# Performance work log

Measured on AMD Instinct MI355X. Metric: run time of the kernel, lower is better.

The kernel has to match this reference:

```python
import jax, jax.numpy as jnp
import numpy as np

D_MODEL = 1024
NUM_HEADS = 16
D_K = D_MODEL // NUM_HEADS
BATCH = 4
SEQ = 1024
NEG_INF = jnp.float32(-1e30)


def setup_inputs() -> dict:
    key = jax.random.key(0)
    ks = jax.random.split(key, 12)
    s = 1.0 / np.sqrt(D_MODEL)
    inp = {
        "Q": jax.random.normal(ks[0], (BATCH, SEQ, D_MODEL), jnp.float32),
        "K": jax.random.normal(ks[1], (BATCH, SEQ, D_MODEL), jnp.float32),
        "V": jax.random.normal(ks[2], (BATCH, SEQ, D_MODEL), jnp.float32),
        # causal mask, broadcastable [1,1,Sq,Sk]; entries==0 are masked out
        "mask": jnp.tril(jnp.ones((SEQ, SEQ), jnp.int32))[None, None],
        "W_q": jax.random.normal(ks[3], (D_MODEL, D_MODEL), jnp.float32) * s,
        "b_q": jnp.zeros((D_MODEL,), jnp.float32),
        "W_k": jax.random.normal(ks[4], (D_MODEL, D_MODEL), jnp.float32) * s,
        "b_k": jnp.zeros((D_MODEL,), jnp.float32),
        "W_v": jax.random.normal(ks[5], (D_MODEL, D_MODEL), jnp.float32) * s,
        "b_v": jnp.zeros((D_MODEL,), jnp.float32),
        "W_o": jax.random.normal(ks[6], (D_MODEL, D_MODEL), jnp.float32) * s,
        "b_o": jnp.zeros((D_MODEL,), jnp.float32),
    }
    return inp


def _split_heads(x):
    b, s, _ = x.shape
    return x.reshape(b, s, NUM_HEADS, D_K).transpose(0, 2, 1, 3)  # [b,h,s,dk]


def reference(Q, K, V, mask, W_q, b_q, W_k, b_k, W_v, b_v, W_o, b_o):
    # linear projections (torch Linear: x @ W.T + b)
    q = _split_heads(Q @ W_q.T + b_q)
    k = _split_heads(K @ W_k.T + b_k)
    v = _split_heads(V @ W_v.T + b_v)
    scale = 1.0 / jnp.sqrt(jnp.float32(D_K))
    scores = jnp.einsum("bhqd,bhkd->bhqk", q, k) * scale
    scores = jnp.where(mask == 0, NEG_INF, scores)
    attn = jax.nn.softmax(scores, axis=-1)  # dropout is identity in eval mode
    out = jnp.einsum("bhqk,bhkd->bhqd", attn, v)
    out = out.transpose(0, 2, 1, 3).reshape(Q.shape[0], Q.shape[1], D_MODEL)
    out = out @ W_o.T + b_o
    return out, attn
```

## Files before the change

kernel.cpp:

```cpp
#include <hip/hip_runtime.h>
#include <math.h>

#define SEQ 1024
#define DM  1024

typedef unsigned short u16;
typedef __attribute__((ext_vector_type(8))) short bf16x8;
typedef __attribute__((ext_vector_type(8))) unsigned short u16x8;
typedef __attribute__((ext_vector_type(4))) float f32x4;

__device__ __forceinline__ u16 f2bf(float f) {
  union { float f; unsigned int u; } x; x.f = f;
  return (u16)((x.u + 0x7fffu + ((x.u >> 16) & 1u)) >> 16);
}

__device__ __forceinline__ void gload16(const void* g, void* l) {
  __builtin_amdgcn_global_load_lds(
      (const __attribute__((address_space(1))) unsigned int*)g,
      (__attribute__((address_space(3))) unsigned int*)l, 16, 0, 0);
}

struct ConvArgs { const float* s[7]; u16* d[7]; };

__global__ __launch_bounds__(256) void conv_bf16(ConvArgs a) {
  const long long t  = (long long)blockIdx.x * 256 + threadIdx.x;
  const long long e0 = t * 8;
  const int u   = (int)(e0 >> 20);
  const int seg = (u < 12) ? (u >> 2) : (u - 9);
  const long long base = (u < 12) ? ((long long)(u >> 2) << 22) : ((long long)u << 20);
  const long long off  = e0 - base;
  const float* sp = a.s[seg] + off;
  float4 x = *(const float4*)sp;
  float4 y = *(const float4*)(sp + 4);
  u16x8 o;
  o[0]=f2bf(x.x); o[1]=f2bf(x.y); o[2]=f2bf(x.z); o[3]=f2bf(x.w);
  o[4]=f2bf(y.x); o[5]=f2bf(y.y); o[6]=f2bf(y.z); o[7]=f2bf(y.w);
  *(u16x8*)(a.d[seg] + off) = o;
}

struct GemmJob  { const u16* X; const u16* W; const float* bias; void* out; int mode; float scale; };
struct GemmJobs { GemmJob j[3]; };

__global__ __launch_bounds__(256) void gemm_bt(GemmJobs jobs) {
  __shared__ u16 As[8192];
  __shared__ u16 Bs[8192];
  const GemmJob job = jobs.j[blockIdx.z];
  const int tid  = threadIdx.x;
  const int wave = tid >> 6, lane = tid & 63;
  const int lm = lane & 15, qd = lane >> 4;
  const int wm = wave & 1,  wn = wave >> 1;
  const int tm = blockIdx.x * 128, tn = blockIdx.y * 128;

  f32x4 acc[4][4];
  #pragma unroll
  for (int i = 0; i < 4; i++)
    #pragma unroll
    for (int jx = 0; jx < 4; jx++) { f32x4 z = {0.f,0.f,0.f,0.f}; acc[i][jx] = z; }

  for (int kt = 0; kt < 1024; kt += 64) {
    #pragma unroll
    for (int i = 0; i < 4; i++) {
      const int s = (wave * 4 + i) * 64 + lane;
      const int r = s >> 3;
      const int c = (s & 7) ^ (r & 7);
      gload16(job.X + (size_t)(tm + r) * 1024 + kt + c * 8, As + (wave * 4 + i) * 512);
      gload16(job.W + (size_t)(tn + r) * 1024 + kt + c * 8, Bs + (wave * 4 + i) * 512);
    }
    __syncthreads();
    #pragma unroll
    for (int ks = 0; ks < 2; ks++) {
      bf16x8 af[4], bf[4];
      #pragma unroll
      for (int i = 0; i < 4; i++) {
        const int ra = wm * 64 + i * 16 + lm;
        af[i] = *(const bf16x8*)&As[ra * 64 + ((((ks << 2) | qd)) ^ (ra & 7)) * 8];
        const int rb = wn * 64 + i * 16 + lm;
        bf[i] = *(const bf16x8*)&Bs[rb * 64 + ((((ks << 2) | qd)) ^ (rb & 7)) * 8];
      }
      #pragma unroll
      for (int mi = 0; mi < 4; mi++)
        #pragma unroll
        for (int ni = 0; ni < 4; ni++)
          acc[mi][ni] = __builtin_amdgcn_mfma_f32_16x16x32_bf16(af[mi], bf[ni], acc[mi][ni], 0, 0, 0);
    }
    __syncthreads();
  }

  #pragma unroll
  for (int ni = 0; ni < 4; ni++) {
    const int n = tn + wn * 64 + ni * 16 + lm;
    const float bn = job.bias[n];
    #pragma unroll
    for (int mi = 0; mi < 4; mi++) {
      #pragma unroll
      for (int r = 0; r < 4; r++) {
        const int m = tm + wm * 64 + mi * 16 + (qd << 2) + r;
        const float v = (acc[mi][ni][r] + bn) * job.scale;
        if (job.mode == 0) {
          const int b = m >> 10, s = m & 1023, h = n >> 6, d = n & 63;
          ((u16*)job.out)[((size_t)((b << 4) + h) * 1024 + s) * 64 + d] = f2bf(v);
        } else if (job.mode == 1) {
          const int b = m >> 10, s = m & 1023, h = n >> 6, d = n & 63;
          ((u16*)job.out)[((size_t)((b << 4) + h) * 64 + d) * 1024 + s] = f2bf(v);
        } else {
          ((float*)job.out)[(size_t)m * 1024 + n] = v;
        }
      }
    }
  }
}

__global__ __launch_bounds__(256)
void attn_pass1(const u16* __restrict__ qbuf, const u16* __restrict__ kbuf,
                const u16* __restrict__ vtbuf, float* __restrict__ Linv,
                u16* __restrict__ ctx, float* __restrict__ attn) {
  __shared__ u16 P[4][512];
  const int tid = threadIdx.x, wave = tid >> 6, lane = tid & 63;
  const int bh = blockIdx.y;

  if (blockIdx.x >= 16) {
    const int b  = blockIdx.x - 16;
    const int L4 = (15 - b) * 16;
    float* base = attn + (size_t)bh * SEQ * SEQ + (size_t)(b * 64) * SEQ + (b + 1) * 64;
    const f32x4 z = {0.f, 0.f, 0.f, 0.f};
    for (int r = 0; r < 64; ++r) {
      f32x4* rowp = (f32x4*)(base + (size_t)r * SEQ);
      for (int s = tid; s < L4; s += 256) rowp[s] = z;
    }
    return;
  }

  const int lm = lane & 15, qd = lane >> 4;
  const int qt = blockIdx.x * 4 + wave;
  const int q0 = qt * 16;
  const u16* Q  = qbuf  + (size_t)bh * SEQ * 64;
  const u16* K  = kbuf  + (size_t)bh * SEQ * 64;
  const u16* VT = vtbuf + (size_t)bh * 64 * SEQ;

  const bf16x8 qa = *(const bf16x8*)(Q + (size_t)(q0 + lm) * 64 + qd * 8);
  const bf16x8 qb = *(const bf16x8*)(Q + (size_t)(q0 + lm) * 64 + 32 + qd * 8);

  f32x4 o[4];
  float lsum[4] = {0.f, 0.f, 0.f, 0.f};
  #pragma unroll
  for (int i = 0; i < 4; i++) { f32x4 z = {0.f,0.f,0.f,0.f}; o[i] = z; }
  u16* Pw = P[wave];

  for (int kt = 0; kt < q0 + 16; kt += 32) {
    const u16* k0p = K + (size_t)(kt + lm) * 64 + qd * 8;
    const u16* k1p = K + (size_t)(kt + 16 + lm) * 64 + qd * 8;
    const bf16x8 k0a = *(const bf16x8*)k0p;
    const bf16x8 k0b = *(const bf16x8*)(k0p + 32);
    const bf16x8 k1a = *(const bf16x8*)k1p;
    const bf16x8 k1b = *(const bf16x8*)(k1p + 32);
    f32x4 s0 = {0.f,0.f,0.f,0.f}, s1 = {0.f,0.f,0.f,0.f};
    s0 = __builtin_amdgcn_mfma_f32_16x16x32_bf16(qa, k0a, s0, 0, 0, 0);
    s0 = __builtin_amdgcn_mfma_f32_16x16x32_bf16(qb, k0b, s0, 0, 0, 0);
    s1 = __builtin_amdgcn_mfma_f32_16x16x32_bf16(qa, k1a, s1, 0, 0, 0);
    s1 = __builtin_amdgcn_mfma_f32_16x16x32_bf16(qb, k1b, s1, 0, 0, 0);
    #pragma unroll
    for (int r = 0; r < 4; r++) {
      const int row = q0 + (qd << 2) + r;
      const float e0 = (kt + lm      <= row) ? __expf(s0[r]) : 0.f;
      const float e1 = (kt + 16 + lm <= row) ? __expf(s1[r]) : 0.f;
      lsum[r] += e0 + e1;
      Pw[((qd << 2) + r) * 32 + lm]      = f2bf(e0);
      Pw[((qd << 2) + r) * 32 + 16 + lm] = f2bf(e1);
    }
    const bf16x8 pf = *(const bf16x8*)&Pw[lm * 32 + qd * 8];
    #pragma unroll
    for (int db = 0; db < 4; db++) {
      const bf16x8 vf = *(const bf16x8*)(VT + (size_t)(db * 16 + lm) * SEQ + kt + qd * 8);
      o[db] = __builtin_amdgcn_mfma_f32_16x16x32_bf16(pf, vf, o[db], 0, 0, 0);
    }
  }

  const int b = bh >> 4, h = bh & 15;
  #pragma unroll
  for (int r = 0; r < 4; r++) {
    float l = lsum[r];
    l += __shfl_xor(l, 1, 16);
    l += __shfl_xor(l, 2, 16);
    l += __shfl_xor(l, 4, 16);
    l += __shfl_xor(l, 8, 16);
    const float inv = 1.0f / l;
    const int row = q0 + (qd << 2) + r;
    if (lm == 0) Linv[(size_t)bh * SEQ + row] = inv;
    #pragma unroll
    for (int db = 0; db < 4; db++) {
      const int d = db * 16 + lm;
      ctx[(size_t)(b * SEQ + row) * DM + h * 64 + d] = f2bf(o[db][r] * inv);
    }
  }
}

__global__ __launch_bounds__(256)
void attn_pass2(const u16* __restrict__ qbuf, const u16* __restrict__ kbuf,
                const float* __restrict__ Linv, float* __restrict__ attn) {
  const int tid = threadIdx.x, wave = tid >> 6, lane = tid & 63;
  const int lm = lane & 15, qd = lane >> 4;
  const int bh = blockIdx.z;
  const int q0 = blockIdx.y * 64;
  const int k0 = blockIdx.x * 256 + wave * 64;
  float* A = attn + (size_t)bh * SEQ * SEQ;

  if (k0 > q0 + 63) {
    const f32x4 z = {0.f,0.f,0.f,0.f};
    #pragma unroll
    for (int i = 0; i < 16; i++)
      *(f32x4*)&A[(size_t)(q0 + i * 4 + qd) * SEQ + k0 + lm * 4] = z;
    return;
  }

  const u16* Q = qbuf + (size_t)bh * SEQ * 64;
  const u16* K = kbuf + (size_t)bh * SEQ * 64;
  bf16x8 qf[4][2]; float invl[4];
  #pragma unroll
  for (int qs = 0; qs < 4; qs++) {
    const int qq = q0 + qs * 16;
    qf[qs][0] = *(const bf16x8*)(Q + (size_t)(qq + lm) * 64 + qd * 8);
    qf[qs][1] = *(const bf16x8*)(Q + (size_t)(qq + lm) * 64 + 32 + qd * 8);
    invl[qs]  = Linv[(size_t)bh * SEQ + qq + lm];
  }
  for (int ks = 0; ks < 4; ks++) {
    const int kk = k0 + ks * 16;
    const u16* kp = K + (size_t)(kk + lm) * 64 + qd * 8;
    const bf16x8 kf0 = *(const bf16x8*)kp;
    const bf16x8 kf1 = *(const bf16x8*)(kp + 32);
    #pragma unroll
    for (int qs = 0; qs < 4; qs++) {
      const int qq = q0 + qs * 16;
      const int kbase = kk + (qd << 2);
      f32x4 v = {0.f,0.f,0.f,0.f};
      if (kk <= qq + 15) {
        f32x4 c = {0.f,0.f,0.f,0.f};
        c = __builtin_amdgcn_mfma_f32_16x16x32_bf16(kf0, qf[qs][0], c, 0, 0, 0);
        c = __builtin_amdgcn_mfma_f32_16x16x32_bf16(kf1, qf[qs][1], c, 0, 0, 0);
        const int qg = qq + lm;
        #pragma unroll
        for (int r = 0; r < 4; r++)
          v[r] = (kbase + r <= qg) ? __expf(c[r]) * invl[qs] : 0.f;
      }
      *(f32x4*)&A[(size_t)(qq + lm) * SEQ + kbase] = v;
    }
  }
}

__global__ __launch_bounds__(256)
void gemmo_pass2(const u16* __restrict__ ctx, const u16* __restrict__ Wob,
                 const float* __restrict__ bo, float* __restrict__ out,
                 const u16* __restrict__ qbuf, const u16* __restrict__ kbuf,
                 const float* __restrict__ Linv, float* __restrict__ attn) {
  __shared__ u16 As[8192];
  __shared__ u16 Bs[8192];
  const int bid = blockIdx.x;
  const int tid = threadIdx.x, wave = tid >> 6, lane = tid & 63;
  const int lm = lane & 15, qd = lane >> 4;

  if (bid < 256) {
    const int wm = wave & 1, wn = wave >> 1;
    const int tm = (bid & 31) * 128, tn = (bid >> 5) * 128;

    f32x4 acc[4][4];
    #pragma unroll
    for (int i = 0; i < 4; i++)
      #pragma unroll
      for (int jx = 0; jx < 4; jx++) { f32x4 z = {0.f,0.f,0.f,0.f}; acc[i][jx] = z; }

    for (int kt = 0; kt < 1024; kt += 64) {
      #pragma unroll
      for (int i = 0; i < 4; i++) {
        const int s = (wave * 4 + i) * 64 + lane;
        const int r = s >> 3;
        const int c = (s & 7) ^ (r & 7);
        gload16(ctx + (size_t)(tm + r) * 1024 + kt + c * 8, As + (wave * 4 + i) * 512);
        gload16(Wob + (size_t)(tn + r) * 1024 + kt + c * 8, Bs + (wave * 4 + i) * 512);
      }
      __syncthreads();
      #pragma unroll
      for (int ks = 0; ks < 2; ks++) {
        bf16x8 af[4], bf[4];
        #pragma unroll
        for (int i = 0; i < 4; i++) {
          const int ra = wm * 64 + i * 16 + lm;
          af[i] = *(const bf16x8*)&As[ra * 64 + ((((ks << 2) | qd)) ^ (ra & 7)) * 8];
          const int rb = wn * 64 + i * 16 + lm;
          bf[i] = *(const bf16x8*)&Bs[rb * 64 + ((((ks << 2) | qd)) ^ (rb & 7)) * 8];
        }
        #pragma unroll
        for (int mi = 0; mi < 4; mi++)
          #pragma unroll
          for (int ni = 0; ni < 4; ni++)
            acc[mi][ni] = __builtin_amdgcn_mfma_f32_16x16x32_bf16(af[mi], bf[ni], acc[mi][ni], 0, 0, 0);
      }
      __syncthreads();
    }

    #pragma unroll
    for (int ni = 0; ni < 4; ni++) {
      const int n = tn + wn * 64 + ni * 16 + lm;
      const float bn = bo[n];
      #pragma unroll
      for (int mi = 0; mi < 4; mi++) {
        #pragma unroll
        for (int r = 0; r < 4; r++) {
          const int m = tm + wm * 64 + mi * 16 + (qd << 2) + r;
          out[(size_t)m * 1024 + n] = acc[mi][ni][r] + bn;
        }
      }
    }
    return;
  }

  const int p  = bid - 256;
  const int bh = p >> 6;
  const int q0 = ((p >> 2) & 15) * 64;
  const int k0 = (p & 3) * 256 + wave * 64;
  float* A = attn + (size_t)bh * SEQ * SEQ;

  if (k0 > q0 + 63) return;

  const u16* Q = qbuf + (size_t)bh * SEQ * 64;
  const u16* K = kbuf + (size_t)bh * SEQ * 64;
  bf16x8 qf[4][2]; float invl[4];
  #pragma unroll
  for (int qs = 0; qs < 4; qs++) {
    const int qq = q0 + qs * 16;
    qf[qs][0] = *(const bf16x8*)(Q + (size_t)(qq + lm) * 64 + qd * 8);
    qf[qs][1] = *(const bf16x8*)(Q + (size_t)(qq + lm) * 64 + 32 + qd * 8);
    invl[qs]  = Linv[(size_t)bh * SEQ + qq + lm];
  }
  for (int ks = 0; ks < 4; ks++) {
    const int kk = k0 + ks * 16;
    const u16* kp = K + (size_t)(kk + lm) * 64 + qd * 8;
    const bf16x8 kf0 = *(const bf16x8*)kp;
    const bf16x8 kf1 = *(const bf16x8*)(kp + 32);
    #pragma unroll
    for (int qs = 0; qs < 4; qs++) {
      const int qq = q0 + qs * 16;
      const int kbase = kk + (qd << 2);
      f32x4 v = {0.f,0.f,0.f,0.f};
      if (kk <= qq + 15) {
        f32x4 c = {0.f,0.f,0.f,0.f};
        c = __builtin_amdgcn_mfma_f32_16x16x32_bf16(kf0, qf[qs][0], c, 0, 0, 0);
        c = __builtin_amdgcn_mfma_f32_16x16x32_bf16(kf1, qf[qs][1], c, 0, 0, 0);
        const int qg = qq + lm;
        #pragma unroll
        for (int r = 0; r < 4; r++)
          v[r] = (kbase + r <= qg) ? __expf(c[r]) * invl[qs] : 0.f;
      }
      *(f32x4*)&A[(size_t)(qq + lm) * SEQ + kbase] = v;
    }
  }
}

extern "C" void kernel_launch(void* const* d_in, const int* in_sizes, int n_in,
                              void* d_out, int out_size, void* d_ws, size_t ws_size,
                              hipStream_t stream)
{
  (void)in_sizes; (void)n_in; (void)out_size;
  const float* Qf = (const float*)d_in[0];
  const float* Kf = (const float*)d_in[1];
  const float* Vf = (const float*)d_in[2];
  const float* Wq = (const float*)d_in[4];
  const float* bq = (const float*)d_in[5];
  const float* Wk = (const float*)d_in[6];
  const float* bk = (const float*)d_in[7];
  const float* Wv = (const float*)d_in[8];
  const float* bv = (const float*)d_in[9];
  const float* Wo = (const float*)d_in[10];
  const float* bo = (const float*)d_in[11];

  float* out  = (float*)d_out;
  float* attn = out + (size_t)4 * SEQ * DM;

  char* sc = (char*)attn;
  u16* Xq  = (u16*)(sc);
  u16* Xk  = (u16*)(sc + (8  << 20));
  u16* Xv  = (u16*)(sc + (16 << 20));
  u16* Wqb = (u16*)(sc + (24 << 20));
  u16* Wkb = (u16*)(sc + (26 << 20));
  u16* Wvb = (u16*)(sc + (28 << 20));
  u16* Wob_sc = (u16*)(sc + (30 << 20));

  char* ws   = (char*)d_ws;
  u16* qbuf  = (u16*)ws;
  u16* kbuf  = (u16*)(ws + (8  << 20));
  u16* vtbuf = (u16*)(ws + (16 << 20));
  float* Linv = (float*)(ws + (24 << 20));

  const int big_ws = ws_size >= ((size_t)35 << 20);
  u16* ctx = big_ws ? (u16*)(ws + (25 << 20)) : (u16*)(sc + (32 << 20));
  u16* Wob = big_ws ? (u16*)(ws + (33 << 20)) : Wob_sc;

  ConvArgs ca;
  ca.s[0]=Qf; ca.s[1]=Kf; ca.s[2]=Vf; ca.s[3]=Wq; ca.s[4]=Wk; ca.s[5]=Wv; ca.s[6]=Wo;
  ca.d[0]=Xq; ca.d[1]=Xk; ca.d[2]=Xv; ca.d[3]=Wqb; ca.d[4]=Wkb; ca.d[5]=Wvb; ca.d[6]=Wob;
  conv_bf16<<<8192, 256, 0, stream>>>(ca);

  GemmJobs gj;
  gj.j[0] = (GemmJob){Xq, Wqb, bq, (void*)qbuf,  0, 0.125f};
  gj.j[1] = (GemmJob){Xk, Wkb, bk, (void*)kbuf,  0, 1.0f};
  gj.j[2] = (GemmJob){Xv, Wvb, bv, (void*)vtbuf, 1, 1.0f};
  gemm_bt<<<dim3(32, 8, 3), 256, 0, stream>>>(gj);

  attn_pass1<<<dim3(big_ws ? 31 : 16, 64), 256, 0, stream>>>(
      qbuf, kbuf, vtbuf, Linv, ctx, attn);

  if (big_ws) {
    gemmo_pass2<<<4352, 256, 0, stream>>>(ctx, Wob, bo, out, qbuf, kbuf, Linv, attn);
  } else {
    GemmJobs go;
    go.j[0] = (GemmJob){ctx, Wob, bo, (void*)out, 2, 1.0f};
    go.j[1] = go.j[0];
    go.j[2] = go.j[0];
    gemm_bt<<<dim3(32, 8, 1), 256, 0, stream>>>(go);
    attn_pass2<<<dim3(4, 16, 64), 256, 0, stream>>>(qbuf, kbuf, Linv, attn);
  }
}
```

Measured before the change: 550.0 us.

## Fold causal zero-band fill of attn into QKV projection GEMM launch

The zero-filling of the masked upper-triangle bands of the attention matrix moves out of attn_pass1 and into extra blocks of the QKV projection GEMM. Those blocks can then overlap with the compute-bound GEMM tiles instead of competing with the attention blocks. To make this legal, the bf16 activation copies are relocated into the workspace and the bf16 weights into the output buffer, so nothing in the attn region is overwritten while it is still being read. The fused path only runs when the workspace is at least 59 MB. In the fallback path the output GEMM now launches 768 blocks that repeat identical work three times.

Result: slower. 572.3 us (+4.0%).

```diff
diff --git a/kernel.cpp b/kernel.cpp
--- a/kernel.cpp
+++ b/kernel.cpp
@@ -41,15 +41,31 @@
 struct GemmJob  { const u16* X; const u16* W; const float* bias; void* out; int mode; float scale; };
 struct GemmJobs { GemmJob j[3]; };
 
-__global__ __launch_bounds__(256) void gemm_bt(GemmJobs jobs) {
+__global__ __launch_bounds__(256) void gemm_bt(GemmJobs jobs, float* attn) {
   __shared__ u16 As[8192];
   __shared__ u16 Bs[8192];
-  const GemmJob job = jobs.j[blockIdx.z];
-  const int tid  = threadIdx.x;
+  const int bid = blockIdx.x;
+  const int tid = threadIdx.x;
+
+  if (bid >= 768) {
+    const int u  = bid - 768;
+    const int bh = u / 15, b = u - bh * 15;
+    const int L4 = (15 - b) * 16;
+    float* base = attn + (size_t)bh * SEQ * SEQ + (size_t)(b * 64) * SEQ + (b + 1) * 64;
+    const f32x4 z = {0.f, 0.f, 0.f, 0.f};
+    for (int r = 0; r < 64; ++r) {
+      f32x4* rowp = (f32x4*)(base + (size_t)r * SEQ);
+      for (int s = tid; s < L4; s += 256) rowp[s] = z;
+    }
+    return;
+  }
+
+  const GemmJob job = jobs.j[bid >> 8];
+  const int rem = bid & 255;
   const int wave = tid >> 6, lane = tid & 63;
   const int lm = lane & 15, qd = lane >> 4;
   const int wm = wave & 1,  wn = wave >> 1;
-  const int tm = blockIdx.x * 128, tn = blockIdx.y * 128;
+  const int tm = (rem & 31) * 128, tn = (rem >> 5) * 128;
 
   f32x4 acc[4][4];
   #pragma unroll
@@ -113,25 +129,12 @@
 __global__ __launch_bounds__(256)
 void attn_pass1(const u16* __restrict__ qbuf, const u16* __restrict__ kbuf,
                 const u16* __restrict__ vtbuf, float* __restrict__ Linv,
-                u16* __restrict__ ctx, float* __restrict__ attn) {
+                u16* __restrict__ ctx) {
   __shared__ u16 P[4][512];
   const int tid = threadIdx.x, wave = tid >> 6, lane = tid & 63;
-  const int bh = blockIdx.y;
-
-  if (blockIdx.x >= 16) {
-    const int b  = blockIdx.x - 16;
-    const int L4 = (15 - b) * 16;
-    float* base = attn + (size_t)bh * SEQ * SEQ + (size_t)(b * 64) * SEQ + (b + 1) * 64;
-    const f32x4 z = {0.f, 0.f, 0.f, 0.f};
-    for (int r = 0; r < 64; ++r) {
-      f32x4* rowp = (f32x4*)(base + (size_t)r * SEQ);
-      for (int s = tid; s < L4; s += 256) rowp[s] = z;
-    }
-    return;
-  }
-
   const int lm = lane & 15, qd = lane >> 4;
   const int qt = blockIdx.x * 4 + wave;
+  const int bh = blockIdx.y;
   const int q0 = qt * 16;
   const u16* Q  = qbuf  + (size_t)bh * SEQ * 64;
   const u16* K  = kbuf  + (size_t)bh * SEQ * 64;
@@ -374,14 +377,15 @@
   float* out  = (float*)d_out;
   float* attn = out + (size_t)4 * SEQ * DM;
 
+  char* ob = (char*)out;
+  u16* Wqb = (u16*)(ob);
+  u16* Wkb = (u16*)(ob + (2 << 20));
+  u16* Wvb = (u16*)(ob + (4 << 20));
+  u16* Wob_sc = (u16*)((char*)attn + (30 << 20));
   char* sc = (char*)attn;
   u16* Xq  = (u16*)(sc);
   u16* Xk  = (u16*)(sc + (8  << 20));
   u16* Xv  = (u16*)(sc + (16 << 20));
-  u16* Wqb = (u16*)(sc + (24 << 20));
-  u16* Wkb = (u16*)(sc + (26 << 20));
-  u16* Wvb = (u16*)(sc + (28 << 20));
-  u16* Wob_sc = (u16*)(sc + (30 << 20));
 
   char* ws   = (char*)d_ws;
   u16* qbuf  = (u16*)ws;
@@ -393,6 +397,14 @@
   u16* ctx = big_ws ? (u16*)(ws + (25 << 20)) : (u16*)(sc + (32 << 20));
   u16* Wob = big_ws ? (u16*)(ws + (33 << 20)) : Wob_sc;
 
+  const int xl_ws = ws_size >= ((size_t)59 << 20);
+  if (xl_ws) {
+    Xq = (u16*)(ws + (35 << 20));
+    Xk = (u16*)(ws + (43 << 20));
+    Xv = (u16*)(ws + (51 << 20));
+  }
+  const int bands_in_gemm = big_ws && xl_ws;
+
   ConvArgs ca;
   ca.s[0]=Qf; ca.s[1]=Kf; ca.s[2]=Vf; ca.s[3]=Wq; ca.s[4]=Wk; ca.s[5]=Wv; ca.s[6]=Wo;
   ca.d[0]=Xq; ca.d[1]=Xk; ca.d[2]=Xv; ca.d[3]=Wqb; ca.d[4]=Wkb; ca.d[5]=Wvb; ca.d[6]=Wob;
@@ -402,19 +414,27 @@
   gj.j[0] = (GemmJob){Xq, Wqb, bq, (void*)qbuf,  0, 0.125f};
   gj.j[1] = (GemmJob){Xk, Wkb, bk, (void*)kbuf,  0, 1.0f};
   gj.j[2] = (GemmJob){Xv, Wvb, bv, (void*)vtbuf, 1, 1.0f};
-  gemm_bt<<<dim3(32, 8, 3), 256, 0, stream>>>(gj);
-
-  attn_pass1<<<dim3(big_ws ? 31 : 16, 64), 256, 0, stream>>>(
-      qbuf, kbuf, vtbuf, Linv, ctx, attn);
+  gemm_bt<<<bands_in_gemm ? 1728 : 768, 256, 0, stream>>>(gj, attn);
+
+  attn_pass1<<<dim3(16, 64), 256, 0, stream>>>(qbuf, kbuf, vtbuf, Linv, ctx);
 
   if (big_ws) {
-    gemmo_pass2<<<4352, 256, 0, stream>>>(ctx, Wob, bo, out, qbuf, kbuf, Linv, attn);
+    if (!bands_in_gemm) {
+      attn_pass2<<<dim3(4, 16, 64), 256, 0, stream>>>(qbuf, kbuf, Linv, attn);
+      GemmJobs go;
+      go.j[0] = (GemmJob){ctx, Wob, bo, (void*)out, 2, 1.0f};
+      go.j[1] = go.j[0];
+      go.j[2] = go.j[0];
+      gemm_bt<<<768, 256, 0, stream>>>(go, attn);
+    } else {
+      gemmo_pass2<<<4352, 256, 0, stream>>>(ctx, Wob, bo, out, qbuf, kbuf, Linv, attn);
+    }
   } else {
     GemmJobs go;
     go.j[0] = (GemmJob){ctx, Wob, bo, (void*)out, 2, 1.0f};
     go.j[1] = go.j[0];
     go.j[2] = go.j[0];
-    gemm_bt<<<dim3(32, 8, 1), 256, 0, stream>>>(go);
+    gemm_bt<<<768, 256, 0, stream>>>(go, attn);
     attn_pass2<<<dim3(4, 16, 64), 256, 0, stream>>>(qbuf, kbuf, Linv, attn);
   }
 }
```

## Overlap masked attn zero-fill with QKV projection GEMM using extra blocks

Applied to the files above, without the earlier changes.

Turns the QKV projection GEMM grid into 1D and, when the workspace is large, appends 870 blocks that zero the masked upper-triangular attention tiles for heads 6..63. To keep those attn regions free, the bf16 Q/K/V weight copies move into the output buffer. attn_pass1 then only zero-fills heads 0..5. The aim is to fill idle CUs during the 768-block GEMM with memory-bound zeroing. The cost is more register and control overhead in the GEMM kernel and more complex buffer aliasing.

Result: no change. 547.8 us, median of 2 (-0.4%).

```diff
diff --git a/kernel.cpp b/kernel.cpp
--- a/kernel.cpp
+++ b/kernel.cpp
@@ -41,15 +41,31 @@
 struct GemmJob  { const u16* X; const u16* W; const float* bias; void* out; int mode; float scale; };
 struct GemmJobs { GemmJob j[3]; };
 
-__global__ __launch_bounds__(256) void gemm_bt(GemmJobs jobs) {
+__global__ __launch_bounds__(256) void gemm_bt(GemmJobs jobs, float* attn) {
   __shared__ u16 As[8192];
   __shared__ u16 Bs[8192];
-  const GemmJob job = jobs.j[blockIdx.z];
-  const int tid  = threadIdx.x;
+  const int bid = blockIdx.x;
+  const int tid = threadIdx.x;
+
+  if (bid >= 768) {
+    const int u  = bid - 768;
+    const int bh = 6 + u / 15, b = u - (bh - 6) * 15;
+    const int L4 = (15 - b) * 16;
+    float* base = attn + (size_t)bh * SEQ * SEQ + (size_t)(b * 64) * SEQ + (b + 1) * 64;
+    const f32x4 z = {0.f, 0.f, 0.f, 0.f};
+    for (int r = 0; r < 64; ++r) {
+      f32x4* rowp = (f32x4*)(base + (size_t)r * SEQ);
+      for (int s = tid; s < L4; s += 256) rowp[s] = z;
+    }
+    return;
+  }
+
+  const GemmJob job = jobs.j[bid >> 8];
+  const int rem = bid & 255;
   const int wave = tid >> 6, lane = tid & 63;
   const int lm = lane & 15, qd = lane >> 4;
   const int wm = wave & 1,  wn = wave >> 1;
-  const int tm = blockIdx.x * 128, tn = blockIdx.y * 128;
+  const int tm = (rem & 31) * 128, tn = (rem >> 5) * 128;
 
   f32x4 acc[4][4];
   #pragma unroll
@@ -119,6 +135,7 @@
   const int bh = blockIdx.y;
 
   if (blockIdx.x >= 16) {
+    if (bh >= 6) return;
     const int b  = blockIdx.x - 16;
     const int L4 = (15 - b) * 16;
     float* base = attn + (size_t)bh * SEQ * SEQ + (size_t)(b * 64) * SEQ + (b + 1) * 64;
@@ -375,15 +392,13 @@
   float* attn = out + (size_t)4 * SEQ * DM;
 
   char* sc = (char*)attn;
-  u16* Xq  = (u16*)(sc);
-  u16* Xk  = (u16*)(sc + (8  << 20));
-  u16* Xv  = (u16*)(sc + (16 << 20));
-  u16* Wqb = (u16*)(sc + (24 << 20));
-  u16* Wkb = (u16*)(sc + (26 << 20));
-  u16* Wvb = (u16*)(sc + (28 << 20));
-  u16* Wob_sc = (u16*)(sc + (30 << 20));
-
-  char* ws   = (char*)d_ws;
+  char* ob = (char*)out;
+  char* ws = (char*)d_ws;
+
+  u16* Xq = (u16*)(sc);
+  u16* Xk = (u16*)(sc + (8  << 20));
+  u16* Xv = (u16*)(sc + (16 << 20));
+
   u16* qbuf  = (u16*)ws;
   u16* kbuf  = (u16*)(ws + (8  << 20));
   u16* vtbuf = (u16*)(ws + (16 << 20));
@@ -391,7 +406,10 @@
 
   const int big_ws = ws_size >= ((size_t)35 << 20);
   u16* ctx = big_ws ? (u16*)(ws + (25 << 20)) : (u16*)(sc + (32 << 20));
-  u16* Wob = big_ws ? (u16*)(ws + (33 << 20)) : Wob_sc;
+  u16* Wob = big_ws ? (u16*)(ws + (33 << 20)) : (u16*)(sc + (30 << 20));
+  u16* Wqb = big_ws ? (u16*)(ob)              : (u16*)(sc + (24 << 20));
+  u16* Wkb = big_ws ? (u16*)(ob + (2 << 20))  : (u16*)(sc + (26 << 20));
+  u16* Wvb = big_ws ? (u16*)(ob + (4 << 20))  : (u16*)(sc + (28 << 20));
 
   ConvArgs ca;
   ca.s[0]=Qf; ca.s[1]=Kf; ca.s[2]=Vf; ca.s[3]=Wq; ca.s[4]=Wk; ca.s[5]=Wv; ca.s[6]=Wo;
@@ -402,7 +420,7 @@
   gj.j[0] = (GemmJob){Xq, Wqb, bq, (void*)qbuf,  0, 0.125f};
   gj.j[1] = (GemmJob){Xk, Wkb, bk, (void*)kbuf,  0, 1.0f};
   gj.j[2] = (GemmJob){Xv, Wvb, bv, (void*)vtbuf, 1, 1.0f};
-  gemm_bt<<<dim3(32, 8, 3), 256, 0, stream>>>(gj);
+  gemm_bt<<<big_ws ? 1638 : 768, 256, 0, stream>>>(gj, attn);
 
   attn_pass1<<<dim3(big_ws ? 31 : 16, 64), 256, 0, stream>>>(
       qbuf, kbuf, vtbuf, Linv, ctx, attn);
@@ -414,7 +432,7 @@
     go.j[0] = (GemmJob){ctx, Wob, bo, (void*)out, 2, 1.0f};
     go.j[1] = go.j[0];
     go.j[2] = go.j[0];
-    gemm_bt<<<dim3(32, 8, 1), 256, 0, stream>>>(go);
+    gemm_bt<<<256, 256, 0, stream>>>(go, attn);
     attn_pass2<<<dim3(4, 16, 64), 256, 0, stream>>>(qbuf, kbuf, Linv, attn);
   }
 }
```
